# Kernel tuning notes

Measured on AMD Instinct MI355X. Metric: run time of the kernel, lower is better.

## Reference

```python
import jax, jax.numpy as jnp
import numpy as np

TAU = 0.1
NEG_EUCLID_DIST = 5.0
COS_EPS = 1e-8


def setup_inputs() -> dict:
    key = jax.random.key(0)
    k1, k2, k3, k4 = jax.random.split(key, 4)
    bs, N, F, S = 4, 8192, 512, 2048
    velo_feat = jax.random.normal(k1, (bs, N, F), dtype=jnp.float32)
    # points in a ~100m cube so the 5m negative-distance mask is a mix of True/False
    velo_pts = jax.random.uniform(k2, (bs, N, 3), dtype=jnp.float32) * 100.0
    ref_feat = jax.random.normal(k3, (bs, N, F), dtype=jnp.float32)
    matches = jax.random.randint(k4, (bs, S, 2), 0, N, dtype=jnp.int64)
    return {"velo_feat": velo_feat, "velo_pts": velo_pts, "ref_feat": ref_feat, "matches": matches}


def _gather(x, idx, width):
    # x: [bs, N, width], idx: [bs, S, 1] -> [bs, S, width]
    bs, S, _ = idx.shape
    return jnp.take_along_axis(x, jnp.broadcast_to(idx, (bs, S, width)), axis=1)


def reference(velo_feat, velo_pts, ref_feat, matches):
    bs, _, F = velo_feat.shape
    anchor_feat = _gather(velo_feat, matches[..., 0:1], F)   # [bs,S,F]
    anchor_pts = _gather(velo_pts, matches[..., 0:1], 3)     # [bs,S,3]
    pos_feat = _gather(ref_feat, matches[..., 1:2], F)       # [bs,S,F]

    # cosine similarity (torch: dot / clamp(|a|*|b|, eps))
    dot = jnp.sum(anchor_feat * pos_feat, axis=-1)
    norms = jnp.linalg.norm(anchor_feat, axis=-1) * jnp.linalg.norm(pos_feat, axis=-1)
    d_pos = (dot / jnp.maximum(norms, COS_EPS))[..., None]   # [bs,S,1]

    # raw (unnormalized) similarity matrix
    D = jnp.einsum('bsf,btf->bst', anchor_feat, pos_feat)    # [bs,S,S]
    D_cat = jnp.concatenate([d_pos, D], axis=2)              # [bs,S,S+1]

    # squared pairwise distance; compare against r^2 (equiv to cdist > r, avoids sqrt)
    sq = jnp.sum(anchor_pts * anchor_pts, axis=-1)           # [bs,S]
    d2 = sq[:, :, None] + sq[:, None, :] - 2.0 * jnp.einsum('bsd,btd->bst', anchor_pts, anchor_pts)
    far = d2 > NEG_EUCLID_DIST * NEG_EUCLID_DIST             # [bs,S,S] bool
    neg_mask = jnp.concatenate([jnp.ones_like(far[:, :, :1]), far], axis=-1)

    denom = jnp.sum(jnp.exp(D_cat / TAU) * neg_mask, axis=-1, keepdims=True)
    loss = -jnp.log(jnp.exp(d_pos / TAU) / denom)            # [bs,S,1]
    return loss.mean()
```

## Files before the change

### kernel.cpp

```cpp
#include <hip/hip_runtime.h>
#include <hip/hip_bf16.h>
#include <cmath>

#define BS 4
#define NP 8192
#define FD 512
#define SM 2048
#define LOG2E10 14.4269504088896340736f
#define LN2 0.6931471805599453f

typedef __attribute__((ext_vector_type(8))) short short8;
typedef __attribute__((ext_vector_type(4))) float f32x4;

static __device__ __forceinline__ unsigned short f2bf(float f) {
  unsigned u = __float_as_uint(f);
  unsigned r = u + 0x7fffu + ((u >> 16) & 1u);
  return (unsigned short)(r >> 16);
}
static __device__ __forceinline__ ushort4 f2bf4(float4 v) {
  ushort4 o;
  o.x = f2bf(v.x); o.y = f2bf(v.y); o.z = f2bf(v.z); o.w = f2bf(v.w);
  return o;
}

__global__ __launch_bounds__(256) void stats_k(
    const float* __restrict__ velo_feat, const float* __restrict__ velo_pts,
    const float* __restrict__ ref_feat, const int* __restrict__ matches,
    float4* __restrict__ pts4, float* __restrict__ dpos,
    unsigned short* __restrict__ Abf, unsigned short* __restrict__ Pbf)
{
  const int row = blockIdx.x * 4 + (threadIdx.x >> 6);
  const int lane = threadIdx.x & 63;
  const int b = row >> 11;
  const int ai = matches[2 * row + 0];
  const int pi = matches[2 * row + 1];

  const float4* ar = (const float4*)(velo_feat + ((size_t)b * NP + ai) * FD);
  const float4* pr = (const float4*)(ref_feat + ((size_t)b * NP + pi) * FD);
  float4 a0 = ar[lane], a1 = ar[lane + 64];
  float4 p0 = pr[lane], p1 = pr[lane + 64];

  *(ushort4*)(Abf + (size_t)row * FD + lane * 4) = f2bf4(a0);
  *(ushort4*)(Abf + (size_t)row * FD + 256 + lane * 4) = f2bf4(a1);
  *(ushort4*)(Pbf + (size_t)row * FD + lane * 4) = f2bf4(p0);
  *(ushort4*)(Pbf + (size_t)row * FD + 256 + lane * 4) = f2bf4(p1);

  float dot = a0.x * p0.x + a0.y * p0.y + a0.z * p0.z + a0.w * p0.w +
              a1.x * p1.x + a1.y * p1.y + a1.z * p1.z + a1.w * p1.w;
  float na = a0.x * a0.x + a0.y * a0.y + a0.z * a0.z + a0.w * a0.w +
             a1.x * a1.x + a1.y * a1.y + a1.z * a1.z + a1.w * a1.w;
  float nb = p0.x * p0.x + p0.y * p0.y + p0.z * p0.z + p0.w * p0.w +
             p1.x * p1.x + p1.y * p1.y + p1.z * p1.z + p1.w * p1.w;
#pragma unroll
  for (int off = 32; off; off >>= 1) {
    dot += __shfl_xor(dot, off);
    na += __shfl_xor(na, off);
    nb += __shfl_xor(nb, off);
  }
  if (lane == 0) {
    dpos[row] = dot / fmaxf(sqrtf(na) * sqrtf(nb), 1e-8f);
    const float* pp = velo_pts + ((size_t)b * NP + ai) * 3;
    float x = pp[0], y = pp[1], z = pp[2];
    pts4[row] = make_float4(x, y, z, x * x + y * y + z * z);
  }
}

__global__ __launch_bounds__(256) void tile_k(
    const unsigned short* __restrict__ Abf, const unsigned short* __restrict__ Pbf,
    const float4* __restrict__ pts4,
    float* __restrict__ maxs, float* __restrict__ sums)
{
  __shared__ unsigned short As[2][8192];
  __shared__ unsigned short Bs[2][8192];

  const int ctile = blockIdx.x, stile = blockIdx.y, b = blockIdx.z;
  const int s0 = stile * 128, c0 = ctile * 128;
  const int tid = threadIdx.x;
  const int wid = tid >> 6, lane = tid & 63;
  const int wr = wid >> 1, wc = wid & 1;
  const int cg = lane >> 4, cr = lane & 15;

  const char* Ab = (const char*)(Abf + ((size_t)b * SM + s0) * FD);
  const char* Bb = (const char*)(Pbf + ((size_t)b * SM + c0) * FD);

  int srow[4], soff[4];
#pragma unroll
  for (int i = 0; i < 4; i++) {
    const int L = (wid * 4 + i) * 1024 + lane * 16;
    srow[i] = L >> 7;
    soff[i] = (L & 127) ^ ((srow[i] & 7) << 4);
  }

#define STAGE(buf, kk)                                                         \
  do {                                                                         \
    _Pragma("unroll") for (int i = 0; i < 4; i++) {                            \
      const int chunk = wid * 4 + i;                                           \
      __builtin_amdgcn_global_load_lds(                                        \
          (const __attribute__((address_space(1))) void*)(                     \
              Ab + ((size_t)srow[i] << 10) + (kk) + soff[i]),                  \
          (__attribute__((address_space(3))) void*)(&As[buf][chunk * 512]),    \
          16, 0, 0);                                                           \
      __builtin_amdgcn_global_load_lds(                                        \
          (const __attribute__((address_space(1))) void*)(                     \
              Bb + ((size_t)srow[i] << 10) + (kk) + soff[i]),                  \
          (__attribute__((address_space(3))) void*)(&Bs[buf][chunk * 512]),    \
          16, 0, 0);                                                           \
    }                                                                          \
  } while (0)

  f32x4 acc[4][4];
#pragma unroll
  for (int n = 0; n < 4; n++)
#pragma unroll
    for (int m = 0; m < 4; m++) acc[n][m] = (f32x4){0.f, 0.f, 0.f, 0.f};

  STAGE(0, 0);
  __syncthreads();

  for (int t = 0; t < 8; ++t) {
    if (t < 7) STAGE((t + 1) & 1, (t + 1) * 128);
    const unsigned short* Asb = As[t & 1];
    const unsigned short* Bsb = Bs[t & 1];
#pragma unroll
    for (int ks = 0; ks < 2; ks++) {
      short8 af[4], bfr[4];
#pragma unroll
      for (int m = 0; m < 4; m++) {
        const int r = wr * 64 + m * 16 + cr;
        const int x = (ks * 64 + cg * 16) ^ ((r & 7) << 4);
        af[m] = *(const short8*)((const char*)Asb + r * 128 + x);
      }
#pragma unroll
      for (int n = 0; n < 4; n++) {
        const int r = wc * 64 + n * 16 + cr;
        const int x = (ks * 64 + cg * 16) ^ ((r & 7) << 4);
        bfr[n] = *(const short8*)((const char*)Bsb + r * 128 + x);
      }
#pragma unroll
      for (int n = 0; n < 4; n++)
#pragma unroll
        for (int m = 0; m < 4; m++)
          acc[n][m] = __builtin_amdgcn_mfma_f32_16x16x32_bf16(bfr[n], af[m],
                                                              acc[n][m], 0, 0, 0);
    }
    if (t < 7) __syncthreads();
  }

  const float4* rpg = pts4 + (size_t)b * SM + s0 + wr * 64;
  const float4* cpg = pts4 + (size_t)b * SM + c0 + wc * 64;
  float4 rv[4];
#pragma unroll
  for (int m = 0; m < 4; m++) rv[m] = rpg[m * 16 + cr];

  float mx[4] = {-INFINITY, -INFINITY, -INFINITY, -INFINITY};
#pragma unroll
  for (int n = 0; n < 4; n++) {
#pragma unroll
    for (int reg = 0; reg < 4; reg++) {
      float4 cv = cpg[n * 16 + cg * 4 + reg];
#pragma unroll
      for (int m = 0; m < 4; m++) {
        float dot = rv[m].x * cv.x + rv[m].y * cv.y + rv[m].z * cv.z;
        float d2 = rv[m].w + cv.w - 2.f * dot;
        float l = (d2 > 25.f) ? acc[n][m][reg] * LOG2E10 : -INFINITY;
        acc[n][m][reg] = l;
        mx[m] = fmaxf(mx[m], l);
      }
    }
  }
  float mxc[4], sm[4];
#pragma unroll
  for (int m = 0; m < 4; m++) {
    mx[m] = fmaxf(mx[m], __shfl_xor(mx[m], 16));
    mx[m] = fmaxf(mx[m], __shfl_xor(mx[m], 32));
    mxc[m] = fmaxf(mx[m], -1e37f);
    sm[m] = 0.f;
  }
#pragma unroll
  for (int n = 0; n < 4; n++)
#pragma unroll
    for (int reg = 0; reg < 4; reg++)
#pragma unroll
      for (int m = 0; m < 4; m++)
        sm[m] += exp2f(acc[n][m][reg] - mxc[m]);
#pragma unroll
  for (int m = 0; m < 4; m++) {
    sm[m] += __shfl_xor(sm[m], 16);
    sm[m] += __shfl_xor(sm[m], 32);
  }
  if (cg == 0) {
    const int ct32 = ctile * 2 + wc;
    size_t base = ((size_t)ct32 * BS + b) * SM + s0 + wr * 64;
#pragma unroll
    for (int m = 0; m < 4; m++) {
      maxs[base + m * 16 + cr] = mx[m];
      sums[base + m * 16 + cr] = sm[m];
    }
  }
#undef STAGE
}

__global__ __launch_bounds__(256) void rowloss_k(
    const float* __restrict__ dpos, const float* __restrict__ maxs,
    const float* __restrict__ sums, double* __restrict__ partial)
{
  const int r = blockIdx.x * 256 + threadIdx.x;
  float l0 = dpos[r] * LOG2E10;
  float M = l0;
#pragma unroll 8
  for (int c = 0; c < 32; c++) M = fmaxf(M, maxs[(size_t)c * BS * SM + r]);
  float s = exp2f(l0 - M);
#pragma unroll 8
  for (int c = 0; c < 32; c++) {
    float mc = maxs[(size_t)c * BS * SM + r];
    float sc = sums[(size_t)c * BS * SM + r];
    s += sc * exp2f(mc - M);
  }
  double v = (double)(LN2 * (M + log2f(s) - l0));
#pragma unroll
  for (int off = 32; off; off >>= 1) v += __shfl_down(v, off);
  __shared__ double red[4];
  if ((threadIdx.x & 63) == 0) red[threadIdx.x >> 6] = v;
  __syncthreads();
  if (threadIdx.x == 0)
    partial[blockIdx.x] = red[0] + red[1] + red[2] + red[3];
}

__global__ __launch_bounds__(64) void final_k(const double* __restrict__ partial,
                                              float* __restrict__ out)
{
  const int t = threadIdx.x;
  double v = (t < 32) ? partial[t] : 0.0;
#pragma unroll
  for (int off = 32; off; off >>= 1) v += __shfl_down(v, off);
  if (t == 0) out[0] = (float)(v / (double)(BS * SM));
}

extern "C" void kernel_launch(void* const* d_in, const int* in_sizes, int n_in,
                              void* d_out, int out_size, void* d_ws, size_t ws_size,
                              hipStream_t stream)
{
  const float* velo_feat = (const float*)d_in[0];
  const float* velo_pts  = (const float*)d_in[1];
  const float* ref_feat  = (const float*)d_in[2];
  const int*   matches   = (const int*)d_in[3];

  char* ws = (char*)d_ws;
  const size_t NBF = (size_t)BS * SM * FD * 2;
  unsigned short* Abf = (unsigned short*)ws;
  unsigned short* Pbf = (unsigned short*)(ws + NBF);
  float4* pts4 = (float4*)(ws + 2 * NBF);
  float*  dpos = (float*)(ws + 2 * NBF + (size_t)BS * SM * 16);
  float*  maxs = (float*)(ws + 2 * NBF + (size_t)BS * SM * 20);
  float*  sums = (float*)(ws + 2 * NBF + (size_t)BS * SM * 20 + (size_t)32 * BS * SM * 4);
  double* partial = (double*)(ws + 2 * NBF + (size_t)BS * SM * 20 + (size_t)64 * BS * SM * 4);

  stats_k<<<BS * SM / 4, 256, 0, stream>>>(velo_feat, velo_pts, ref_feat,
                                           matches, pts4, dpos, Abf, Pbf);
  tile_k<<<dim3(16, 16, BS), 256, 0, stream>>>(Abf, Pbf, pts4, maxs, sums);
  rowloss_k<<<BS * SM / 256, 256, 0, stream>>>(dpos, maxs, sums, partial);
  final_k<<<1, 64, 0, stream>>>(partial, (float*)d_out);
}
```

Baseline: 73.42 us.

## Enlarge GEMM tile to 256x256 with 8 waves and fine-grained staged pipeline

The similarity tile kernel moves from 128x128 tiles with 4 waves to 256x256 tiles with 8 waves, so each wave computes 128x64 outputs. The K loop is split into half-steps whose global-to-LDS loads are interleaved with MFMA groups under explicit vmcnt/lgkmcnt waits, barriers and setprio. The grid is flattened with a remapped block index so neighbouring blocks share operand tiles in cache. This aims to raise operand reuse and overlap memory with compute, at the cost of more registers, more LDS (64KB) and only 256 blocks on a 256-CU device.

```diff
diff --git a/kernel.cpp b/kernel.cpp
--- a/kernel.cpp
+++ b/kernel.cpp
@@ -65,101 +65,157 @@
   }
 }
 
-__global__ __launch_bounds__(256) void tile_k(
+__global__ __launch_bounds__(512) void tile_k(
     const unsigned short* __restrict__ Abf, const unsigned short* __restrict__ Pbf,
     const float4* __restrict__ pts4,
     float* __restrict__ maxs, float* __restrict__ sums)
 {
-  __shared__ unsigned short As[2][8192];
-  __shared__ unsigned short Bs[2][8192];
-
-  const int ctile = blockIdx.x, stile = blockIdx.y, b = blockIdx.z;
-  const int s0 = stile * 128, c0 = ctile * 128;
+  __shared__ unsigned short As[2][2][8192];
+  __shared__ unsigned short Bs[2][2][8192];
+
+  const int wg = ((blockIdx.x & 7) << 5) + (blockIdx.x >> 3);
+  const int b = wg >> 6;
+  const int stile = (wg >> 3) & 7;
+  const int ctile = wg & 7;
+  const int s0 = stile * 256, c0 = ctile * 256;
+
   const int tid = threadIdx.x;
   const int wid = tid >> 6, lane = tid & 63;
-  const int wr = wid >> 1, wc = wid & 1;
+  const int wr = wid >> 2, wc = wid & 3;
   const int cg = lane >> 4, cr = lane & 15;
 
   const char* Ab = (const char*)(Abf + ((size_t)b * SM + s0) * FD);
   const char* Bb = (const char*)(Pbf + ((size_t)b * SM + c0) * FD);
 
-  int srow[4], soff[4];
-#pragma unroll
-  for (int i = 0; i < 4; i++) {
-    const int L = (wid * 4 + i) * 1024 + lane * 16;
-    srow[i] = L >> 7;
-    soff[i] = (L & 127) ^ ((srow[i] & 7) << 4);
-  }
-
-#define STAGE(buf, kk)                                                         \
-  do {                                                                         \
-    _Pragma("unroll") for (int i = 0; i < 4; i++) {                            \
-      const int chunk = wid * 4 + i;                                           \
-      __builtin_amdgcn_global_load_lds(                                        \
-          (const __attribute__((address_space(1))) void*)(                     \
-              Ab + ((size_t)srow[i] << 10) + (kk) + soff[i]),                  \
-          (__attribute__((address_space(3))) void*)(&As[buf][chunk * 512]),    \
-          16, 0, 0);                                                           \
-      __builtin_amdgcn_global_load_lds(                                        \
-          (const __attribute__((address_space(1))) void*)(                     \
-              Bb + ((size_t)srow[i] << 10) + (kk) + soff[i]),                  \
-          (__attribute__((address_space(3))) void*)(&Bs[buf][chunk * 512]),    \
-          16, 0, 0);                                                           \
-    }                                                                          \
+  int srcoff[2];
+#pragma unroll
+  for (int i = 0; i < 2; i++) {
+    const int L = i * 8192 + tid * 16;
+    const int q = L >> 7;
+    const int inner = (L & 127) ^ ((q & 7) << 4);
+    const int r = (q << 1) | (inner >> 6);
+    const int c = inner & 63;
+    srcoff[i] = r * (FD * 2) + c;
+  }
+
+#define STAGEH(X, Xb, kt, kh, bufi)                                           \
+  do {                                                                        \
+    _Pragma("unroll") for (int i = 0; i < 2; i++) {                           \
+      __builtin_amdgcn_global_load_lds(                                       \
+          (const __attribute__((address_space(1))) void*)(                    \
+              Xb + srcoff[i] + (kt) * 128 + (kh) * 64),                       \
+          (__attribute__((address_space(3))) void*)(                          \
+              (char*)&X[bufi][kh][0] + i * 8192 + wid * 1024),                \
+          16, 0, 0);                                                          \
+    }                                                                         \
   } while (0)
 
-  f32x4 acc[4][4];
+#define WAITDS()                                          \
+  do {                                                    \
+    asm volatile("s_waitcnt lgkmcnt(0)" ::: "memory");    \
+    __builtin_amdgcn_sched_barrier(0);                    \
+  } while (0)
+
+#define BAR()                                             \
+  do {                                                    \
+    __builtin_amdgcn_s_barrier();                         \
+    __builtin_amdgcn_sched_barrier(0);                    \
+  } while (0)
+
+  f32x4 acc[4][8];
 #pragma unroll
   for (int n = 0; n < 4; n++)
 #pragma unroll
-    for (int m = 0; m < 4; m++) acc[n][m] = (f32x4){0.f, 0.f, 0.f, 0.f};
-
-  STAGE(0, 0);
-  __syncthreads();
-
-  for (int t = 0; t < 8; ++t) {
-    if (t < 7) STAGE((t + 1) & 1, (t + 1) * 128);
-    const unsigned short* Asb = As[t & 1];
-    const unsigned short* Bsb = Bs[t & 1];
-#pragma unroll
-    for (int ks = 0; ks < 2; ks++) {
-      short8 af[4], bfr[4];
-#pragma unroll
-      for (int m = 0; m < 4; m++) {
-        const int r = wr * 64 + m * 16 + cr;
-        const int x = (ks * 64 + cg * 16) ^ ((r & 7) << 4);
-        af[m] = *(const short8*)((const char*)Asb + r * 128 + x);
-      }
-#pragma unroll
-      for (int n = 0; n < 4; n++) {
-        const int r = wc * 64 + n * 16 + cr;
-        const int x = (ks * 64 + cg * 16) ^ ((r & 7) << 4);
-        bfr[n] = *(const short8*)((const char*)Bsb + r * 128 + x);
-      }
-#pragma unroll
-      for (int n = 0; n < 4; n++)
-#pragma unroll
-        for (int m = 0; m < 4; m++)
-          acc[n][m] = __builtin_amdgcn_mfma_f32_16x16x32_bf16(bfr[n], af[m],
-                                                              acc[n][m], 0, 0, 0);
-    }
-    if (t < 7) __syncthreads();
-  }
-
-  const float4* rpg = pts4 + (size_t)b * SM + s0 + wr * 64;
+    for (int m = 0; m < 8; m++) acc[n][m] = (f32x4){0.f, 0.f, 0.f, 0.f};
+
+  short8 af[4], bfr[4];
+
+  auto LDB_ = [&](int bufi, int kh) {
+#pragma unroll
+    for (int n = 0; n < 4; n++) {
+      const int r = wc * 64 + n * 16 + cr;
+      const int q = r >> 1;
+      const int v = ((((r & 1) << 6) | (cg << 4)) ^ ((q & 7) << 4));
+      bfr[n] = *(const short8*)((const char*)&Bs[bufi][kh][0] + q * 128 + v);
+    }
+  };
+  auto LDA_ = [&](int bufi, int kh, int mg) {
+#pragma unroll
+    for (int j = 0; j < 4; j++) {
+      const int r = wr * 128 + (mg * 4 + j) * 16 + cr;
+      const int q = r >> 1;
+      const int v = ((((r & 1) << 6) | (cg << 4)) ^ ((q & 7) << 4));
+      af[j] = *(const short8*)((const char*)&As[bufi][kh][0] + q * 128 + v);
+    }
+  };
+  auto MFMA16_ = [&](int mg) {
+    __builtin_amdgcn_s_setprio(1);
+#pragma unroll
+    for (int n = 0; n < 4; n++)
+#pragma unroll
+      for (int j = 0; j < 4; j++)
+        acc[n][mg * 4 + j] = __builtin_amdgcn_mfma_f32_16x16x32_bf16(
+            bfr[n], af[j], acc[n][mg * 4 + j], 0, 0, 0);
+    __builtin_amdgcn_s_setprio(0);
+  };
+
+  STAGEH(As, Ab, 0, 0, 0);
+  STAGEH(Bs, Bb, 0, 0, 0);
+  STAGEH(As, Ab, 0, 1, 0);
+  STAGEH(Bs, Bb, 0, 1, 0);
+
+#pragma unroll 1
+  for (int kt = 0; kt < 8; ++kt) {
+    const int bufi = kt & 1, nbuf = bufi ^ 1;
+    if (kt < 7) {
+      STAGEH(As, Ab, kt + 1, 0, nbuf);
+      asm volatile("s_waitcnt vmcnt(6)" ::: "memory");
+    } else {
+      asm volatile("s_waitcnt vmcnt(4)" ::: "memory");
+    }
+    BAR();
+    LDB_(bufi, 0);
+    LDA_(bufi, 0, 0);
+    WAITDS();
+    MFMA16_(0);
+    if (kt < 7) STAGEH(Bs, Bb, kt + 1, 0, nbuf);
+    LDA_(bufi, 0, 1);
+    WAITDS();
+    MFMA16_(1);
+    if (kt < 7) {
+      STAGEH(As, Ab, kt + 1, 1, nbuf);
+      asm volatile("s_waitcnt vmcnt(6)" ::: "memory");
+    } else {
+      asm volatile("s_waitcnt vmcnt(0)" ::: "memory");
+    }
+    BAR();
+    LDB_(bufi, 1);
+    LDA_(bufi, 1, 0);
+    WAITDS();
+    MFMA16_(0);
+    if (kt < 7) STAGEH(Bs, Bb, kt + 1, 1, nbuf);
+    LDA_(bufi, 1, 1);
+    WAITDS();
+    MFMA16_(1);
+    BAR();
+  }
+
+  const float4* rpg = pts4 + (size_t)b * SM + s0 + wr * 128;
   const float4* cpg = pts4 + (size_t)b * SM + c0 + wc * 64;
-  float4 rv[4];
-#pragma unroll
-  for (int m = 0; m < 4; m++) rv[m] = rpg[m * 16 + cr];
-
-  float mx[4] = {-INFINITY, -INFINITY, -INFINITY, -INFINITY};
+  float4 rv[8];
+#pragma unroll
+  for (int m = 0; m < 8; m++) rv[m] = rpg[m * 16 + cr];
+
+  float mx[8];
+#pragma unroll
+  for (int m = 0; m < 8; m++) mx[m] = -INFINITY;
 #pragma unroll
   for (int n = 0; n < 4; n++) {
 #pragma unroll
     for (int reg = 0; reg < 4; reg++) {
       float4 cv = cpg[n * 16 + cg * 4 + reg];
 #pragma unroll
-      for (int m = 0; m < 4; m++) {
+      for (int m = 0; m < 8; m++) {
         float dot = rv[m].x * cv.x + rv[m].y * cv.y + rv[m].z * cv.z;
         float d2 = rv[m].w + cv.w - 2.f * dot;
         float l = (d2 > 25.f) ? acc[n][m][reg] * LOG2E10 : -INFINITY;
@@ -168,9 +224,9 @@
       }
     }
   }
-  float mxc[4], sm[4];
-#pragma unroll
-  for (int m = 0; m < 4; m++) {
+  float mxc[8], sm[8];
+#pragma unroll
+  for (int m = 0; m < 8; m++) {
     mx[m] = fmaxf(mx[m], __shfl_xor(mx[m], 16));
     mx[m] = fmaxf(mx[m], __shfl_xor(mx[m], 32));
     mxc[m] = fmaxf(mx[m], -1e37f);
@@ -181,23 +237,25 @@
 #pragma unroll
     for (int reg = 0; reg < 4; reg++)
 #pragma unroll
-      for (int m = 0; m < 4; m++)
+      for (int m = 0; m < 8; m++)
         sm[m] += exp2f(acc[n][m][reg] - mxc[m]);
 #pragma unroll
-  for (int m = 0; m < 4; m++) {
+  for (int m = 0; m < 8; m++) {
     sm[m] += __shfl_xor(sm[m], 16);
     sm[m] += __shfl_xor(sm[m], 32);
   }
   if (cg == 0) {
-    const int ct32 = ctile * 2 + wc;
-    size_t base = ((size_t)ct32 * BS + b) * SM + s0 + wr * 64;
-#pragma unroll
-    for (int m = 0; m < 4; m++) {
+    const int ct32 = ctile * 4 + wc;
+    size_t base = ((size_t)ct32 * BS + b) * SM + s0 + wr * 128;
+#pragma unroll
+    for (int m = 0; m < 8; m++) {
       maxs[base + m * 16 + cr] = mx[m];
       sums[base + m * 16 + cr] = sm[m];
     }
   }
-#undef STAGE
+#undef STAGEH
+#undef WAITDS
+#undef BAR
 }
 
 __global__ __launch_bounds__(256) void rowloss_k(
@@ -257,7 +315,7 @@
 
   stats_k<<<BS * SM / 4, 256, 0, stream>>>(velo_feat, velo_pts, ref_feat,
                                            matches, pts4, dpos, Abf, Pbf);
-  tile_k<<<dim3(16, 16, BS), 256, 0, stream>>>(Abf, Pbf, pts4, maxs, sums);
+  tile_k<<<256, 512, 0, stream>>>(Abf, Pbf, pts4, maxs, sums);
   rowloss_k<<<BS * SM / 256, 256, 0, stream>>>(dpos, maxs, sums, partial);
   final_k<<<1, 64, 0, stream>>>(partial, (float*)d_out);
 }
```

New measurement: 75.52 us. 1.03x slower.

## Single-buffer LDS tiles and remap workgroups to XCD-aware order in tile kernel

Applied to the files above, without the earlier changes.

The tile kernel drops its double-buffered LDS staging for a single buffer, synchronizing before and after each K-slice load. Shared memory drops to 32KB, which may raise occupancy per CU. The grid becomes 1D and block IDs are remapped so consecutive tiles of the same batch and row land on the same XCD, which should improve L2 reuse. In exchange, global loads no longer overlap with MFMA work inside a block, so latency hiding now depends on other resident blocks.

```diff
diff --git a/kernel.cpp b/kernel.cpp
--- a/kernel.cpp
+++ b/kernel.cpp
@@ -70,11 +70,15 @@
     const float4* __restrict__ pts4,
     float* __restrict__ maxs, float* __restrict__ sums)
 {
-  __shared__ unsigned short As[2][8192];
-  __shared__ unsigned short Bs[2][8192];
-
-  const int ctile = blockIdx.x, stile = blockIdx.y, b = blockIdx.z;
+  __shared__ unsigned short As[128 * 64];
+  __shared__ unsigned short Bs[128 * 64];
+
+  const int wg = ((blockIdx.x & 7) << 7) + (blockIdx.x >> 3);
+  const int b = wg >> 8;
+  const int stile = (wg >> 4) & 15;
+  const int ctile = wg & 15;
   const int s0 = stile * 128, c0 = ctile * 128;
+
   const int tid = threadIdx.x;
   const int wid = tid >> 6, lane = tid & 63;
   const int wr = wid >> 1, wc = wid & 1;
@@ -91,36 +95,30 @@
     soff[i] = (L & 127) ^ ((srow[i] & 7) << 4);
   }
 
-#define STAGE(buf, kk)                                                         \
-  do {                                                                         \
-    _Pragma("unroll") for (int i = 0; i < 4; i++) {                            \
-      const int chunk = wid * 4 + i;                                           \
-      __builtin_amdgcn_global_load_lds(                                        \
-          (const __attribute__((address_space(1))) void*)(                     \
-              Ab + ((size_t)srow[i] << 10) + (kk) + soff[i]),                  \
-          (__attribute__((address_space(3))) void*)(&As[buf][chunk * 512]),    \
-          16, 0, 0);                                                           \
-      __builtin_amdgcn_global_load_lds(                                        \
-          (const __attribute__((address_space(1))) void*)(                     \
-              Bb + ((size_t)srow[i] << 10) + (kk) + soff[i]),                  \
-          (__attribute__((address_space(3))) void*)(&Bs[buf][chunk * 512]),    \
-          16, 0, 0);                                                           \
-    }                                                                          \
-  } while (0)
-
   f32x4 acc[4][4];
 #pragma unroll
   for (int n = 0; n < 4; n++)
 #pragma unroll
     for (int m = 0; m < 4; m++) acc[n][m] = (f32x4){0.f, 0.f, 0.f, 0.f};
 
-  STAGE(0, 0);
-  __syncthreads();
-
-  for (int t = 0; t < 8; ++t) {
-    if (t < 7) STAGE((t + 1) & 1, (t + 1) * 128);
-    const unsigned short* Asb = As[t & 1];
-    const unsigned short* Bsb = Bs[t & 1];
+  for (int kk = 0; kk < FD * 2; kk += 128) {
+    __syncthreads();
+#pragma unroll
+    for (int i = 0; i < 4; i++) {
+      const int chunk = wid * 4 + i;
+      __builtin_amdgcn_global_load_lds(
+          (const __attribute__((address_space(1))) void*)(
+              Ab + (size_t)srow[i] * (FD * 2) + kk + soff[i]),
+          (__attribute__((address_space(3))) void*)((char*)As + chunk * 1024),
+          16, 0, 0);
+      __builtin_amdgcn_global_load_lds(
+          (const __attribute__((address_space(1))) void*)(
+              Bb + (size_t)srow[i] * (FD * 2) + kk + soff[i]),
+          (__attribute__((address_space(3))) void*)((char*)Bs + chunk * 1024),
+          16, 0, 0);
+    }
+    __syncthreads();
+
 #pragma unroll
     for (int ks = 0; ks < 2; ks++) {
       short8 af[4], bfr[4];
@@ -128,13 +126,13 @@
       for (int m = 0; m < 4; m++) {
         const int r = wr * 64 + m * 16 + cr;
         const int x = (ks * 64 + cg * 16) ^ ((r & 7) << 4);
-        af[m] = *(const short8*)((const char*)Asb + r * 128 + x);
+        af[m] = *(const short8*)((const char*)As + r * 128 + x);
       }
 #pragma unroll
       for (int n = 0; n < 4; n++) {
         const int r = wc * 64 + n * 16 + cr;
         const int x = (ks * 64 + cg * 16) ^ ((r & 7) << 4);
-        bfr[n] = *(const short8*)((const char*)Bsb + r * 128 + x);
+        bfr[n] = *(const short8*)((const char*)Bs + r * 128 + x);
       }
 #pragma unroll
       for (int n = 0; n < 4; n++)
@@ -143,7 +141,6 @@
           acc[n][m] = __builtin_amdgcn_mfma_f32_16x16x32_bf16(bfr[n], af[m],
                                                               acc[n][m], 0, 0, 0);
     }
-    if (t < 7) __syncthreads();
   }
 
   const float4* rpg = pts4 + (size_t)b * SM + s0 + wr * 64;
@@ -197,7 +194,6 @@
       sums[base + m * 16 + cr] = sm[m];
     }
   }
-#undef STAGE
 }
 
 __global__ __launch_bounds__(256) void rowloss_k(
@@ -257,7 +253,7 @@
 
   stats_k<<<BS * SM / 4, 256, 0, stream>>>(velo_feat, velo_pts, ref_feat,
                                            matches, pts4, dpos, Abf, Pbf);
-  tile_k<<<dim3(16, 16, BS), 256, 0, stream>>>(Abf, Pbf, pts4, maxs, sums);
+  tile_k<<<1024, 256, 0, stream>>>(Abf, Pbf, pts4, maxs, sums);
   rowloss_k<<<BS * SM / 256, 256, 0, stream>>>(dpos, maxs, sums, partial);
   final_k<<<1, 64, 0, stream>>>(partial, (float*)d_out);
 }
```

Result: slower. 75.89 us (+3.4%).
